# Performance work log

Hardware: AMD Instinct MI355X
Metric: run time of the kernel (lower is better)

Reference implementation:

```python
import jax, jax.numpy as jnp
import numpy as np

B = 16
NS = [12000, 3000, 750, 188, 47]   # nodes per level
ES = [72000, 18000, 4500, 1128, 282]  # directed edges per level (~6N, mesh)
FL = [3, 32, 64, 128, 128]
WN = 16
Z = 8


def _vco(x, ei, ec, W, b):
    # edge-conditioned conv: x (B,N,Ci), ei (2,E) [src,dst], ec (E,WN), W (WN,Ci,Co)
    src, dst = ei[0], ei[1]
    k = jnp.einsum('ew,wio->eio', ec, W)            # per-edge mixed kernel
    msg = jnp.einsum('bei,eio->beo', x[:, src], k)  # gather + transform
    out = jnp.zeros((x.shape[0], x.shape[1], W.shape[2]), x.dtype)
    out = out.at[:, dst].add(msg)                   # scatter-sum to targets
    return out + b


def _pool(x, m):
    # sparse pool/unpool applied as matmul: (M,N) @ (B,N,C) -> (B,M,C)
    return jnp.einsum('mn,bnc->bmc', m, x)


def setup_inputs():
    key = jax.random.key(0)
    ks = iter(jax.random.split(key, 80))
    d = {'x': jax.random.normal(next(ks), (B, NS[0], FL[0]), jnp.float32)}
    for i in range(5):
        src = jax.random.randint(next(ks), (ES[i],), 0, NS[i])
        dst = jax.random.randint(next(ks), (ES[i],), 0, NS[i])
        d[f'ei{i}'] = jnp.stack([src, dst]).astype(jnp.int32)
        d[f'ec{i}'] = jax.random.normal(next(ks), (ES[i], WN), jnp.float32)
    for i in range(4):
        d[f'Wc{i}'] = jax.random.normal(next(ks), (WN, FL[i], FL[i + 1]), jnp.float32) * 0.1
        d[f'bc{i}'] = jnp.zeros((FL[i + 1],), jnp.float32)
        ci, co = FL[4 - i], FL[3 - i]
        d[f'Wd{i}'] = jax.random.normal(next(ks), (WN, ci, co), jnp.float32) * 0.1
        d[f'bd{i}'] = jnp.zeros((co,), jnp.float32)
        d[f'dm{i}'] = jax.random.normal(next(ks), (NS[i + 1], NS[i]), jnp.float32) * (1.0 / np.sqrt(NS[i]))
        d[f'um{i}'] = jax.random.normal(next(ks), (NS[i], NS[i + 1]), jnp.float32) * (1.0 / np.sqrt(NS[i + 1]))
    d['encW'] = jax.random.normal(next(ks), (Z, NS[4] * FL[4]), jnp.float32) * 0.1
    d['encb'] = jnp.zeros((Z,), jnp.float32)
    d['decW'] = jax.random.normal(next(ks), (FL[4] * NS[4], Z), jnp.float32) * 0.1
    d['decb'] = jnp.zeros((FL[4] * NS[4],), jnp.float32)
    return d


def _forward(x, eis, ecs, Wcs, bcs, Wds, bds, dms, ums, encW, encb, decW, decb):
    # encoder
    for i in range(4):
        x = jax.nn.relu(_vco(x, eis[i], ecs[i], Wcs[i], bcs[i]))
        x = _pool(x, dms[i])
    z = x.reshape(x.shape[0], -1) @ encW.T + encb
    # decoder
    y = (z @ decW.T + decb).reshape(x.shape[0], -1, FL[4])
    for i in range(3):
        y = _pool(y, ums[3 - i])
        y = jax.nn.relu(_vco(y, eis[3 - i], ecs[3 - i], Wds[i], bds[i]))
    y = _pool(y, ums[0])
    return _vco(y, eis[0], ecs[0], Wds[3], bds[3])


def reference(x, ei0, ei1, ei2, ei3, ei4, ec0, ec1, ec2, ec3, ec4,
              Wc0, Wc1, Wc2, Wc3, bc0, bc1, bc2, bc3,
              Wd0, Wd1, Wd2, Wd3, bd0, bd1, bd2, bd3,
              dm0, dm1, dm2, dm3, um0, um1, um2, um3,
              encW, encb, decW, decb):
    return _forward(x, [ei0, ei1, ei2, ei3, ei4], [ec0, ec1, ec2, ec3, ec4],
                    [Wc0, Wc1, Wc2, Wc3], [bc0, bc1, bc2, bc3],
                    [Wd0, Wd1, Wd2, Wd3], [bd0, bd1, bd2, bd3],
                    [dm0, dm1, dm2, dm3], [um0, um1, um2, um3],
                    encW, encb, decW, decb)
```

## Files before the change

kernel.cpp:

```cpp
#include <hip/hip_runtime.h>


typedef __attribute__((ext_vector_type(8))) short bf16x8;
typedef __attribute__((ext_vector_type(4))) float f32x4;

__device__ inline unsigned bf1(float x){
  union {float f; unsigned u;} a; a.f = x;
  return (a.u + 0x7fffu + ((a.u >> 16) & 1u)) >> 16;
}
__device__ inline unsigned pack_bf2(float x, float y){ return bf1(x) | (bf1(y) << 16); }
__device__ inline float2 unp_bf2(unsigned u){
  union {unsigned i; float f;} a, b;
  a.i = u << 16; b.i = u & 0xffff0000u;
  return make_float2(a.f, b.f);
}

__device__ inline void gld_lds16(const void* g, void* l){
  __builtin_amdgcn_global_load_lds((const __attribute__((address_space(1))) void*)g,
                                   (__attribute__((address_space(3))) void*)l, 16, 0, 0);
}

__global__ void k_zero_f32(float* __restrict__ p, int n){
  int i = blockIdx.x * 256 + threadIdx.x; if (i < n) p[i] = 0.f;
}
__global__ void k_zero_i32(int* __restrict__ p, int n){
  int i = blockIdx.x * 256 + threadIdx.x; if (i < n) p[i] = 0;
}
__global__ void k_transpose_in(const float* __restrict__ x, float* __restrict__ xT){
  int gid = blockIdx.x * 256 + threadIdx.x;
  if (gid >= 16 * 12000 * 3) return;
  int b = gid / 36000; int r = gid % 36000; int n = r / 3; int c = r % 3;
  xT[n * 48 + b * 3 + c] = x[gid];
}

__global__ void k_count(const int* __restrict__ ei, int E, int* __restrict__ cnt){
  int e = blockIdx.x * 256 + threadIdx.x;
  if (e < E) atomicAdd(&cnt[ei[E + e]], 1);
}
__global__ void k_scan(int* __restrict__ cnt, int* __restrict__ rowptr, int n){
  __shared__ int s[256];
  __shared__ int carryS;
  int t = threadIdx.x;
  if (t == 0){ carryS = 0; rowptr[0] = 0; }
  __syncthreads();
  for (int base = 0; base < n; base += 256){
    int i = base + t;
    int v = (i < n) ? cnt[i] : 0;
    s[t] = v;
    __syncthreads();
    for (int off = 1; off < 256; off <<= 1){
      int a = (t >= off) ? s[t - off] : 0;
      __syncthreads();
      s[t] += a;
      __syncthreads();
    }
    int carry = carryS;
    int incl = s[t];
    if (i < n){ rowptr[i + 1] = carry + incl; cnt[i] = carry + incl - v; }
    __syncthreads();
    if (t == 255) carryS = carry + s[255];
    __syncthreads();
  }
}
__global__ void k_fill(const int* __restrict__ ei, int E, int* __restrict__ cursor, int* __restrict__ perm){
  int e = blockIdx.x * 256 + threadIdx.x;
  if (e < E){ int p = atomicAdd(&cursor[ei[E + e]], 1); perm[p] = e; }
}

__global__ void k_cvt_pad(const float* __restrict__ in, unsigned short* __restrict__ out,
                          int M, int K, int Kp, int total8){
  int gid = blockIdx.x * 256 + threadIdx.x;
  if (gid >= total8) return;
  int j = gid * 8;
  int row = j / Kp, col = j % Kp;
  float v[8];
  if (row < M && col + 8 <= K && (K & 3) == 0){
    const float* p = in + (size_t)row * K + col;
    float4 x0 = *(const float4*)p;
    float4 x1 = *(const float4*)(p + 4);
    v[0]=x0.x; v[1]=x0.y; v[2]=x0.z; v[3]=x0.w;
    v[4]=x1.x; v[5]=x1.y; v[6]=x1.z; v[7]=x1.w;
  } else {
    #pragma unroll
    for (int c = 0; c < 8; ++c)
      v[c] = (row < M && col + c < K) ? in[(size_t)row * K + col + c] : 0.f;
  }
  uint4 o;
  o.x = pack_bf2(v[0], v[1]); o.y = pack_bf2(v[2], v[3]);
  o.z = pack_bf2(v[4], v[5]); o.w = pack_bf2(v[6], v[7]);
  *(uint4*)(out + (size_t)gid * 8) = o;
}
__global__ void k_cvt_T(const float* __restrict__ in, unsigned short* __restrict__ out,
                        int K, int N, int Kp){
  __shared__ float ts[32][33];
  int t = threadIdx.x;
  int k0 = blockIdx.x * 32, n0 = blockIdx.y * 32;
  #pragma unroll
  for (int rep = 0; rep < 4; ++rep){
    int i = t + rep * 256;
    int kr = i >> 5, nc = i & 31;
    ts[kr][nc] = (k0 + kr < K) ? in[(size_t)(k0 + kr) * N + n0 + nc] : 0.f;
  }
  __syncthreads();
  #pragma unroll
  for (int rep = 0; rep < 4; ++rep){
    int i = t + rep * 256;
    int nr = i >> 5, kc = i & 31;
    out[(size_t)(n0 + nr) * Kp + k0 + kc] = (unsigned short)bf1(ts[kc][nr]);
  }
}

__global__ __launch_bounds__(256) void k_mgemm(const unsigned short* __restrict__ A,
                                               const unsigned short* __restrict__ Bt,
                                               float* __restrict__ C,
                                               int M, int N, int Kp, int Kc, int splitK){
  __shared__ __align__(16) short As[4096];
  __shared__ __align__(16) short Bs[4096];
  int t = threadIdx.x, lane = t & 63, w = t >> 6;
  int n0 = blockIdx.x << 7, m0 = blockIdx.y << 7;
  int k0 = blockIdx.z * Kc;
  int kend = min(Kp, k0 + Kc);
  int s0 = w * 128 + lane, s1 = s0 + 64;
  const unsigned short* gA0 = A + (size_t)(m0 + (s0 & 127)) * Kp + (s0 >> 7) * 8 + k0;
  const unsigned short* gA1 = A + (size_t)(m0 + (s1 & 127)) * Kp + (s1 >> 7) * 8 + k0;
  const unsigned short* gB0 = Bt + (size_t)(n0 + (s0 & 127)) * Kp + (s0 >> 7) * 8 + k0;
  const unsigned short* gB1 = Bt + (size_t)(n0 + (s1 & 127)) * Kp + (s1 >> 7) * 8 + k0;
  short* lA0 = As + (size_t)(w * 128) * 8;
  short* lA1 = As + (size_t)(w * 128 + 64) * 8;
  short* lB0 = Bs + (size_t)(w * 128) * 8;
  short* lB1 = Bs + (size_t)(w * 128 + 64) * 8;
  f32x4 acc[4][4];
  #pragma unroll
  for (int mt = 0; mt < 4; ++mt)
    #pragma unroll
    for (int nt = 0; nt < 4; ++nt){ acc[mt][nt][0]=0.f; acc[mt][nt][1]=0.f; acc[mt][nt][2]=0.f; acc[mt][nt][3]=0.f; }
  int q = lane >> 4, r = lane & 15;
  int mrow = (w >> 1) * 64, nrow = (w & 1) * 64;
  const short* pa = As + (size_t)(q * 128 + mrow + r) * 8;
  const short* pb = Bs + (size_t)(q * 128 + nrow + r) * 8;
  for (int kk = k0; kk < kend; kk += 32){
    gld_lds16(gA0, lA0); gld_lds16(gA1, lA1);
    gld_lds16(gB0, lB0); gld_lds16(gB1, lB1);
    gA0 += 32; gA1 += 32; gB0 += 32; gB1 += 32;
    __syncthreads();
    bf16x8 af[4], bg[4];
    #pragma unroll
    for (int mt = 0; mt < 4; ++mt) af[mt] = *(const bf16x8*)(pa + mt * 128);
    #pragma unroll
    for (int nt = 0; nt < 4; ++nt) bg[nt] = *(const bf16x8*)(pb + nt * 128);
    #pragma unroll
    for (int mt = 0; mt < 4; ++mt)
      #pragma unroll
      for (int nt = 0; nt < 4; ++nt)
        acc[mt][nt] = __builtin_amdgcn_mfma_f32_16x16x32_bf16(af[mt], bg[nt], acc[mt][nt], 0, 0, 0);
    __syncthreads();
  }
  int mb = m0 + mrow + q * 4;
  int nb = n0 + nrow + r;
  #pragma unroll
  for (int mt = 0; mt < 4; ++mt){
    #pragma unroll
    for (int reg = 0; reg < 4; ++reg){
      int m = mb + mt * 16 + reg;
      if (m < M){
        float* cp = C + (size_t)m * N + nb;
        if (splitK > 1){
          #pragma unroll
          for (int nt = 0; nt < 4; ++nt) atomicAdd(cp + nt * 16, acc[mt][nt][reg]);
        } else {
          #pragma unroll
          for (int nt = 0; nt < 4; ++nt) cp[nt * 16] = acc[mt][nt][reg];
        }
      }
    }
  }
}

__global__ __launch_bounds__(256) void k_kmat_big(const float* __restrict__ ec, const float* __restrict__ W,
                                                  unsigned short* __restrict__ kbuf, int E, int CiCo4){
  __shared__ float ecs[128];
  int t = threadIdx.x;
  int e0 = blockIdx.y * 8;
  if (t < 128){ int el = t >> 4, w = t & 15; int e = e0 + el; ecs[t] = (e < E) ? ec[e * 16 + w] : 0.f; }
  __syncthreads();
  int j4 = blockIdx.x * 256 + t;
  const float4* W4 = (const float4*)W;
  float4 w16[16];
  #pragma unroll
  for (int w = 0; w < 16; ++w) w16[w] = W4[(size_t)w * CiCo4 + j4];
  uint2* k2 = (uint2*)kbuf;
  #pragma unroll 1
  for (int el = 0; el < 8; ++el){
    int e = e0 + el; if (e >= E) break;
    float4 a = {0.f, 0.f, 0.f, 0.f};
    #pragma unroll
    for (int w = 0; w < 16; ++w){
      float s = ecs[el * 16 + w];
      a.x += s * w16[w].x; a.y += s * w16[w].y; a.z += s * w16[w].z; a.w += s * w16[w].w;
    }
    k2[(size_t)e * CiCo4 + j4] = make_uint2(pack_bf2(a.x, a.y), pack_bf2(a.z, a.w));
  }
}
__global__ __launch_bounds__(256) void k_kmat_small(const float* __restrict__ ec, const float* __restrict__ W,
                                                    unsigned short* __restrict__ kbuf, int E){
  __shared__ float4 Ws[16 * 24];
  __shared__ float ecs[32 * 16];
  int t = threadIdx.x;
  for (int i = t; i < 384; i += 256) Ws[i] = ((const float4*)W)[i];
  int e0 = blockIdx.x * 32;
  for (int i = t; i < 512; i += 256){ int el = i >> 4, w = i & 15; int e = e0 + el; ecs[i] = (e < E) ? ec[e * 16 + w] : 0.f; }
  __syncthreads();
  int el = t >> 3, jj = t & 7;
  int e = e0 + el;
  if (e >= E) return;
  uint2* k2 = (uint2*)kbuf;
  #pragma unroll 1
  for (int rep = 0; rep < 3; ++rep){
    int j4 = jj + rep * 8;
    float4 a = {0.f, 0.f, 0.f, 0.f};
    #pragma unroll
    for (int w = 0; w < 16; ++w){
      float s = ecs[el * 16 + w];
      float4 wv = Ws[w * 24 + j4];
      a.x += s * wv.x; a.y += s * wv.y; a.z += s * wv.z; a.w += s * wv.w;
    }
    k2[(size_t)e * 24 + j4] = make_uint2(pack_bf2(a.x, a.y), pack_bf2(a.z, a.w));
  }
}

__global__ __launch_bounds__(256) void k_conv_l0_enc(const float* __restrict__ xT, const unsigned short* __restrict__ kbuf,
                                                     const int* __restrict__ ei, const int* __restrict__ rowptr,
                                                     const int* __restrict__ perm, const float* __restrict__ bias,
                                                     float* __restrict__ out){
  int gid = blockIdx.x * 256 + threadIdx.x;
  int n = gid >> 4, b = gid & 15;
  if (n >= 12000) return;
  float acc[32];
  #pragma unroll
  for (int o = 0; o < 32; ++o) acc[o] = 0.f;
  int r1 = rowptr[n + 1];
  for (int r = rowptr[n]; r < r1; ++r){
    int e = perm[r];
    int src = ei[e];
    const float* xp = xT + src * 48 + b * 3;
    float xv[3] = {xp[0], xp[1], xp[2]};
    const uint4* kq = (const uint4*)(kbuf + (size_t)e * 96);
    #pragma unroll
    for (int i = 0; i < 3; ++i){
      #pragma unroll
      for (int o8 = 0; o8 < 4; ++o8){
        uint4 u = kq[i * 4 + o8];
        float2 f0 = unp_bf2(u.x), f1 = unp_bf2(u.y), f2 = unp_bf2(u.z), f3 = unp_bf2(u.w);
        int ob = o8 * 8;
        acc[ob + 0] += xv[i] * f0.x; acc[ob + 1] += xv[i] * f0.y;
        acc[ob + 2] += xv[i] * f1.x; acc[ob + 3] += xv[i] * f1.y;
        acc[ob + 4] += xv[i] * f2.x; acc[ob + 5] += xv[i] * f2.y;
        acc[ob + 6] += xv[i] * f3.x; acc[ob + 7] += xv[i] * f3.y;
      }
    }
  }
  float4* op = (float4*)(out + (size_t)n * 512 + b * 32);
  #pragma unroll
  for (int o4 = 0; o4 < 8; ++o4){
    float4 v;
    v.x = fmaxf(acc[o4 * 4 + 0] + bias[o4 * 4 + 0], 0.f);
    v.y = fmaxf(acc[o4 * 4 + 1] + bias[o4 * 4 + 1], 0.f);
    v.z = fmaxf(acc[o4 * 4 + 2] + bias[o4 * 4 + 2], 0.f);
    v.w = fmaxf(acc[o4 * 4 + 3] + bias[o4 * 4 + 3], 0.f);
    op[o4] = v;
  }
}
__global__ __launch_bounds__(256) void k_conv_l0_dec(const float* __restrict__ xin, const unsigned short* __restrict__ kbuf,
                                                     const int* __restrict__ ei, const int* __restrict__ rowptr,
                                                     const int* __restrict__ perm, const float* __restrict__ bias,
                                                     float* __restrict__ out){
  int gid = blockIdx.x * 256 + threadIdx.x;
  int n = gid >> 4, b = gid & 15;
  if (n >= 12000) return;
  float acc0 = 0.f, acc1 = 0.f, acc2 = 0.f;
  int r1 = rowptr[n + 1];
  for (int r = rowptr[n]; r < r1; ++r){
    int e = perm[r];
    int src = ei[e];
    const float4* xr = (const float4*)(xin + (size_t)src * 512 + b * 32);
    const unsigned* kw = (const unsigned*)(kbuf + (size_t)e * 96);
    #pragma unroll
    for (int c = 0; c < 8; ++c){
      float4 xv = xr[c];
      float2 p0 = unp_bf2(kw[6 * c + 0]);
      float2 p1 = unp_bf2(kw[6 * c + 1]);
      float2 p2 = unp_bf2(kw[6 * c + 2]);
      float2 p3 = unp_bf2(kw[6 * c + 3]);
      float2 p4 = unp_bf2(kw[6 * c + 4]);
      float2 p5 = unp_bf2(kw[6 * c + 5]);
      acc0 += xv.x * p0.x; acc1 += xv.x * p0.y; acc2 += xv.x * p1.x;
      acc0 += xv.y * p1.y; acc1 += xv.y * p2.x; acc2 += xv.y * p2.y;
      acc0 += xv.z * p3.x; acc1 += xv.z * p3.y; acc2 += xv.z * p4.x;
      acc0 += xv.w * p4.y; acc1 += xv.w * p5.x; acc2 += xv.w * p5.y;
    }
  }
  float* op = out + (size_t)b * 36000 + n * 3;
  op[0] = acc0 + bias[0];
  op[1] = acc1 + bias[1];
  op[2] = acc2 + bias[2];
}

template<int CI, int CO, int S, bool RELU>
__global__ __launch_bounds__(256) void k_conv_mid(const float* __restrict__ xin, const unsigned short* __restrict__ kbuf,
                                                  const int* __restrict__ ei, const int* __restrict__ rowptr,
                                                  const int* __restrict__ perm, const float* __restrict__ bias,
                                                  float* __restrict__ out){
  constexpr int COC = CO / S;
  constexpr int V   = COC / 16;
  constexpr int IT  = (CI > 64) ? 64 : CI;
  constexpr int NIH = CI / IT;
  constexpr int COP = COC + 4;
  constexpr int XP  = IT + 4;
  __shared__ float ks[IT * COP];
  __shared__ float xs[16 * XP];
  int n = blockIdx.x, cy = blockIdx.y;
  int ob0 = cy * COC;
  int t = threadIdx.x;
  int og = t >> 4, b = t & 15;
  float acc[V];
  #pragma unroll
  for (int j = 0; j < V; ++j) acc[j] = 0.f;
  int r0 = rowptr[n], r1 = rowptr[n + 1];
  for (int r = r0; r < r1; ++r){
    int e = perm[r];
    int src = ei[e];
    const float4* xbase = (const float4*)(xin + (size_t)src * (16 * CI));
    for (int ih = 0; ih < NIH; ++ih){
      __syncthreads();
      const uint4* kb = (const uint4*)(kbuf + (size_t)e * (CI * CO) + ih * (IT * CO));
      constexpr int KS8 = IT * COC / 8;
      for (int i8 = t; i8 < KS8; i8 += 256){
        int i = (i8 * 8) / COC, o = (i8 * 8) % COC;
        uint4 u = kb[(i * CO + ob0 + o) >> 3];
        float* d = &ks[i * COP + o];
        float2 f0 = unp_bf2(u.x), f1 = unp_bf2(u.y), f2 = unp_bf2(u.z), f3 = unp_bf2(u.w);
        *(float4*)&d[0] = make_float4(f0.x, f0.y, f1.x, f1.y);
        *(float4*)&d[4] = make_float4(f2.x, f2.y, f3.x, f3.y);
      }
      constexpr int XS4 = 16 * IT / 4;
      for (int i4 = t; i4 < XS4; i4 += 256){
        int bb = i4 / (IT / 4), iq = i4 % (IT / 4);
        float4 v = xbase[bb * (CI / 4) + ih * (IT / 4) + iq];
        *(float4*)&xs[bb * XP + iq * 4] = v;
      }
      __syncthreads();
      #pragma unroll 4
      for (int i = 0; i < IT; ++i){
        float xv = xs[b * XP + i];
        if constexpr (V == 8){
          const float4* kp = (const float4*)&ks[i * COP + og * 8];
          float4 p0 = kp[0], p1 = kp[1];
          acc[0] += xv * p0.x; acc[1] += xv * p0.y; acc[2] += xv * p0.z; acc[3] += xv * p0.w;
          acc[4] += xv * p1.x; acc[5] += xv * p1.y; acc[6] += xv * p1.z; acc[7] += xv * p1.w;
        } else if constexpr (V == 4){
          float4 p0 = *(const float4*)&ks[i * COP + og * 4];
          acc[0] += xv * p0.x; acc[1] += xv * p0.y; acc[2] += xv * p0.z; acc[3] += xv * p0.w;
        } else {
          float2 p0 = *(const float2*)&ks[i * COP + og * 2];
          acc[0] += xv * p0.x; acc[1] += xv * p0.y;
        }
      }
    }
  }
  float* op = out + (size_t)n * (16 * CO) + b * CO + ob0 + og * V;
  #pragma unroll
  for (int j = 0; j < V; ++j){
    float v = acc[j] + bias[ob0 + og * V + j];
    if (RELU) v = fmaxf(v, 0.f);
    op[j] = v;
  }
}

__global__ void k_encfc(const float* __restrict__ x, const float* __restrict__ encW,
                        const float* __restrict__ encb, float* __restrict__ z){
  __shared__ float red[128];
  int bq = blockIdx.x; int b = bq >> 3, q = bq & 7;
  int t = threadIdx.x;
  float s = 0.f;
  for (int j = t; j < 6016; j += 128){
    int n = j >> 7, c = j & 127;
    s += x[n * 2048 + b * 128 + c] * encW[q * 6016 + j];
  }
  red[t] = s; __syncthreads();
  for (int o = 64; o > 0; o >>= 1){ if (t < o) red[t] += red[t + o]; __syncthreads(); }
  if (t == 0) z[b * 8 + q] = red[0] + encb[q];
}
__global__ void k_decfc(const float* __restrict__ z, const float* __restrict__ decW,
                        const float* __restrict__ decb, float* __restrict__ y){
  int gid = blockIdx.x * 256 + threadIdx.x;
  if (gid >= 6016 * 16) return;
  int c = gid & 127, bn = gid >> 7; int b = bn & 15, n = bn >> 4;
  int j = n * 128 + c;
  float s = decb[j];
  #pragma unroll
  for (int q = 0; q < 8; ++q) s += z[b * 8 + q] * decW[j * 8 + q];
  y[gid] = s;
}

extern "C" void kernel_launch(void* const* d_in, const int* in_sizes, int n_in,
                              void* d_out, int out_size, void* d_ws, size_t ws_size,
                              hipStream_t stream){
  const float* x   = (const float*)d_in[0];
  const int*   ei0 = (const int*)d_in[1];  const float* ec0 = (const float*)d_in[2];
  const int*   ei1 = (const int*)d_in[3];  const float* ec1 = (const float*)d_in[4];
  const int*   ei2 = (const int*)d_in[5];  const float* ec2 = (const float*)d_in[6];
  const int*   ei3 = (const int*)d_in[7];  const float* ec3 = (const float*)d_in[8];
  const float* Wc0 = (const float*)d_in[11], *bc0 = (const float*)d_in[12];
  const float* Wd0 = (const float*)d_in[13], *bd0 = (const float*)d_in[14];
  const float* dm0 = (const float*)d_in[15], *um0 = (const float*)d_in[16];
  const float* Wc1 = (const float*)d_in[17], *bc1 = (const float*)d_in[18];
  const float* Wd1 = (const float*)d_in[19], *bd1 = (const float*)d_in[20];
  const float* dm1 = (const float*)d_in[21], *um1 = (const float*)d_in[22];
  const float* Wc2 = (const float*)d_in[23], *bc2 = (const float*)d_in[24];
  const float* Wd2 = (const float*)d_in[25], *bd2 = (const float*)d_in[26];
  const float* dm2 = (const float*)d_in[27], *um2 = (const float*)d_in[28];
  const float* Wc3 = (const float*)d_in[29], *bc3 = (const float*)d_in[30];
  const float* Wd3 = (const float*)d_in[31], *bd3 = (const float*)d_in[32];
  const float* dm3 = (const float*)d_in[33], *um3 = (const float*)d_in[34];
  const float* encW = (const float*)d_in[35], *encb = (const float*)d_in[36];
  const float* decW = (const float*)d_in[37], *decb = (const float*)d_in[38];

  char* wsb = (char*)d_ws;
  unsigned short* kbuf = (unsigned short*)wsb;
  unsigned short* Abf  = kbuf;
  float* bufA = (float*)(wsb + 73728000);
  float* bufB = (float*)(wsb + 98304000);
  unsigned short* Bt = (unsigned short*)(wsb + 122880000);
  float* xT   = (float*)(wsb + 135168000);
  float* zb   = (float*)(wsb + 137472000);
  int* ip = (int*)(wsb + 137472512);
  int* cnt0 = ip; ip += 12000;
  int* cnt1 = ip; ip += 3000;
  int* cnt2 = ip; ip += 750;
  int* cnt3 = ip; ip += 188;
  int* row0 = ip; ip += 12001;
  int* row1 = ip; ip += 3001;
  int* row2 = ip; ip += 751;
  int* row3 = ip; ip += 189;
  int* perm0 = ip; ip += 72000;
  int* perm1 = ip; ip += 18000;
  int* perm2 = ip; ip += 4500;
  int* perm3 = ip; ip += 1128;

  dim3 blk(256);
  k_transpose_in<<<2250, blk, 0, stream>>>(x, xT);
  k_zero_i32<<<63, blk, 0, stream>>>(cnt0, 15938);
  k_count<<<282, blk, 0, stream>>>(ei0, 72000, cnt0);
  k_count<<<71,  blk, 0, stream>>>(ei1, 18000, cnt1);
  k_count<<<18,  blk, 0, stream>>>(ei2, 4500, cnt2);
  k_count<<<5,   blk, 0, stream>>>(ei3, 1128, cnt3);
  k_scan<<<1, blk, 0, stream>>>(cnt0, row0, 12000);
  k_scan<<<1, blk, 0, stream>>>(cnt1, row1, 3000);
  k_scan<<<1, blk, 0, stream>>>(cnt2, row2, 750);
  k_scan<<<1, blk, 0, stream>>>(cnt3, row3, 188);
  k_fill<<<282, blk, 0, stream>>>(ei0, 72000, cnt0, perm0);
  k_fill<<<71,  blk, 0, stream>>>(ei1, 18000, cnt1, perm1);
  k_fill<<<18,  blk, 0, stream>>>(ei2, 4500, cnt2, perm2);
  k_fill<<<5,   blk, 0, stream>>>(ei3, 1128, cnt3, perm3);

  k_kmat_small<<<2250, blk, 0, stream>>>(ec0, Wc0, kbuf, 72000);
  k_conv_l0_enc<<<750, blk, 0, stream>>>(xT, kbuf, ei0, row0, perm0, bc0, bufA);
  k_cvt_T<<<dim3(375, 16), blk, 0, stream>>>(bufA, Bt, 12000, 512, 12000);
  k_cvt_pad<<<18000, blk, 0, stream>>>(dm0, Abf, 3000, 12000, 12000, 4608000);
  k_zero_f32<<<6000, blk, 0, stream>>>(bufB, 1536000);
  k_mgemm<<<dim3(4, 24, 12), blk, 0, stream>>>(Abf, Bt, bufB, 3000, 512, 12000, 1024, 12);
  k_kmat_big<<<dim3(2, 2250), blk, 0, stream>>>(ec1, Wc1, kbuf, 18000, 512);
  k_conv_mid<32, 64, 1, true><<<dim3(3000, 1), blk, 0, stream>>>(bufB, kbuf, ei1, row1, perm1, bc1, bufA);
  k_cvt_T<<<dim3(94, 32), blk, 0, stream>>>(bufA, Bt, 3000, 1024, 3008);
  k_cvt_pad<<<1128, blk, 0, stream>>>(dm1, Abf, 750, 3000, 3008, 288768);
  k_zero_f32<<<3000, blk, 0, stream>>>(bufB, 768000);
  k_mgemm<<<dim3(8, 6, 16), blk, 0, stream>>>(Abf, Bt, bufB, 750, 1024, 3008, 192, 16);
  k_kmat_big<<<dim3(8, 563), blk, 0, stream>>>(ec2, Wc2, kbuf, 4500, 2048);
  k_conv_mid<64, 128, 4, true><<<dim3(750, 4), blk, 0, stream>>>(bufB, kbuf, ei2, row2, perm2, bc2, bufA);
  k_cvt_T<<<dim3(24, 64), blk, 0, stream>>>(bufA, Bt, 750, 2048, 768);
  k_cvt_pad<<<96, blk, 0, stream>>>(dm2, Abf, 188, 750, 768, 24576);
  k_zero_f32<<<1504, blk, 0, stream>>>(bufB, 385024);
  k_mgemm<<<dim3(16, 2, 12), blk, 0, stream>>>(Abf, Bt, bufB, 188, 2048, 768, 64, 12);
  k_kmat_big<<<dim3(16, 141), blk, 0, stream>>>(ec3, Wc3, kbuf, 1128, 4096);
  k_conv_mid<128, 128, 4, true><<<dim3(188, 4), blk, 0, stream>>>(bufB, kbuf, ei3, row3, perm3, bc3, bufA);
  k_cvt_T<<<dim3(6, 64), blk, 0, stream>>>(bufA, Bt, 188, 2048, 192);
  k_cvt_pad<<<12, blk, 0, stream>>>(dm3, Abf, 47, 188, 192, 3072);
  k_zero_f32<<<376, blk, 0, stream>>>(bufB, 96256);
  k_mgemm<<<dim3(16, 1, 6), blk, 0, stream>>>(Abf, Bt, bufB, 47, 2048, 192, 32, 6);

  k_encfc<<<128, dim3(128), 0, stream>>>(bufB, encW, encb, zb);
  k_decfc<<<376, blk, 0, stream>>>(zb, decW, decb, bufA);

  k_cvt_T<<<dim3(2, 64), blk, 0, stream>>>(bufA, Bt, 47, 2048, 64);
  k_cvt_pad<<<8, blk, 0, stream>>>(um3, Abf, 188, 47, 64, 2048);
  k_zero_f32<<<1504, blk, 0, stream>>>(bufB, 385024);
  k_mgemm<<<dim3(16, 2, 2), blk, 0, stream>>>(Abf, Bt, bufB, 188, 2048, 64, 32, 2);
  k_kmat_big<<<dim3(16, 141), blk, 0, stream>>>(ec3, Wd0, kbuf, 1128, 4096);
  k_conv_mid<128, 128, 4, true><<<dim3(188, 4), blk, 0, stream>>>(bufB, kbuf, ei3, row3, perm3, bd0, bufA);
  k_cvt_T<<<dim3(6, 64), blk, 0, stream>>>(bufA, Bt, 188, 2048, 192);
  k_cvt_pad<<<72, blk, 0, stream>>>(um2, Abf, 750, 188, 192, 18432);
  k_zero_f32<<<6000, blk, 0, stream>>>(bufB, 1536000);
  k_mgemm<<<dim3(16, 6, 6), blk, 0, stream>>>(Abf, Bt, bufB, 750, 2048, 192, 32, 6);
  k_kmat_big<<<dim3(8, 563), blk, 0, stream>>>(ec2, Wd1, kbuf, 4500, 2048);
  k_conv_mid<128, 64, 2, true><<<dim3(750, 2), blk, 0, stream>>>(bufB, kbuf, ei2, row2, perm2, bd1, bufA);
  k_cvt_T<<<dim3(24, 32), blk, 0, stream>>>(bufA, Bt, 750, 1024, 768);
  k_cvt_pad<<<1152, blk, 0, stream>>>(um1, Abf, 3000, 750, 768, 294912);
  k_zero_f32<<<12000, blk, 0, stream>>>(bufB, 3072000);
  k_mgemm<<<dim3(8, 24, 4), blk, 0, stream>>>(Abf, Bt, bufB, 3000, 1024, 768, 192, 4);
  k_kmat_big<<<dim3(2, 2250), blk, 0, stream>>>(ec1, Wd2, kbuf, 18000, 512);
  k_conv_mid<64, 32, 1, true><<<dim3(3000, 1), blk, 0, stream>>>(bufB, kbuf, ei1, row1, perm1, bd2, bufA);
  k_cvt_T<<<dim3(94, 16), blk, 0, stream>>>(bufA, Bt, 3000, 512, 3008);
  k_cvt_pad<<<17672, blk, 0, stream>>>(um0, Abf, 12000, 3000, 3008, 4524032);
  k_zero_f32<<<24000, blk, 0, stream>>>(bufB, 6144000);
  k_mgemm<<<dim3(4, 94, 4), blk, 0, stream>>>(Abf, Bt, bufB, 12000, 512, 3008, 768, 4);
  k_kmat_small<<<2250, blk, 0, stream>>>(ec0, Wd3, kbuf, 72000);
  k_conv_l0_dec<<<750, blk, 0, stream>>>(bufB, kbuf, ei0, row0, perm0, bd3, (float*)d_out);
}
```

Measured before the change: 1.614 ms.

## Double-buffer GEMM LDS loads, retune split-K, and batch CSR build kernels

The bf16 MFMA GEMM now double-buffers its LDS tiles. The next K-slice's global-to-LDS load is issued before computing on the current one, and one barrier per iteration is dropped. Several split-K factors are lowered and chunk sizes raised, which means fewer atomics and more work per block. The per-level count, scan and fill kernels are merged into three multi-level launches, and the scan now uses wave shuffles instead of a barrier-heavy LDS scan. Costs are doubled LDS per block and less parallelism on some GEMM launches.

```diff
diff --git a/kernel.cpp b/kernel.cpp
--- a/kernel.cpp
+++ b/kernel.cpp
@@ -33,38 +33,66 @@
   xT[n * 48 + b * 3 + c] = x[gid];
 }
 
-__global__ void k_count(const int* __restrict__ ei, int E, int* __restrict__ cnt){
-  int e = blockIdx.x * 256 + threadIdx.x;
-  if (e < E) atomicAdd(&cnt[ei[E + e]], 1);
-}
-__global__ void k_scan(int* __restrict__ cnt, int* __restrict__ rowptr, int n){
-  __shared__ int s[256];
-  __shared__ int carryS;
+__global__ void k_count_all(const int* __restrict__ ei0, const int* __restrict__ ei1,
+                            const int* __restrict__ ei2, const int* __restrict__ ei3,
+                            int* __restrict__ cnt0, int* __restrict__ cnt1,
+                            int* __restrict__ cnt2, int* __restrict__ cnt3){
+  int g = blockIdx.x * 256 + threadIdx.x;
+  const int* ei; int* cnt; int e, E;
+  if (g < 72000){ ei = ei0; cnt = cnt0; e = g; E = 72000; }
+  else if (g < 90000){ ei = ei1; cnt = cnt1; e = g - 72000; E = 18000; }
+  else if (g < 94500){ ei = ei2; cnt = cnt2; e = g - 90000; E = 4500; }
+  else if (g < 95628){ ei = ei3; cnt = cnt3; e = g - 94500; E = 1128; }
+  else return;
+  atomicAdd(&cnt[ei[E + e]], 1);
+}
+__global__ void k_scan_all(int* c0, int* c1, int* c2, int* c3,
+                           int* r0, int* r1, int* r2, int* r3){
+  int lvl = blockIdx.x;
+  int* cnt    = lvl == 0 ? c0 : lvl == 1 ? c1 : lvl == 2 ? c2 : c3;
+  int* rowptr = lvl == 0 ? r0 : lvl == 1 ? r1 : lvl == 2 ? r2 : r3;
+  int n       = lvl == 0 ? 12000 : lvl == 1 ? 3000 : lvl == 2 ? 750 : 188;
   int t = threadIdx.x;
-  if (t == 0){ carryS = 0; rowptr[0] = 0; }
+  int L = (n + 255) / 256;
+  int beg = t * L, end = min(n, beg + L);
+  int s = 0;
+  for (int i = beg; i < end; ++i) s += cnt[i];
+  int lane = t & 63, wv = t >> 6;
+  int incl = s;
+  #pragma unroll
+  for (int d = 1; d < 64; d <<= 1){
+    int v = __shfl_up(incl, d, 64);
+    if (lane >= d) incl += v;
+  }
+  __shared__ int wsum[4];
+  if (lane == 63) wsum[wv] = incl;
   __syncthreads();
-  for (int base = 0; base < n; base += 256){
-    int i = base + t;
-    int v = (i < n) ? cnt[i] : 0;
-    s[t] = v;
-    __syncthreads();
-    for (int off = 1; off < 256; off <<= 1){
-      int a = (t >= off) ? s[t - off] : 0;
-      __syncthreads();
-      s[t] += a;
-      __syncthreads();
-    }
-    int carry = carryS;
-    int incl = s[t];
-    if (i < n){ rowptr[i + 1] = carry + incl; cnt[i] = carry + incl - v; }
-    __syncthreads();
-    if (t == 255) carryS = carry + s[255];
-    __syncthreads();
-  }
-}
-__global__ void k_fill(const int* __restrict__ ei, int E, int* __restrict__ cursor, int* __restrict__ perm){
-  int e = blockIdx.x * 256 + threadIdx.x;
-  if (e < E){ int p = atomicAdd(&cursor[ei[E + e]], 1); perm[p] = e; }
+  int wbase = 0;
+  for (int i = 0; i < wv; ++i) wbase += wsum[i];
+  int run = wbase + incl - s;
+  for (int i = beg; i < end; ++i){
+    int v = cnt[i];
+    cnt[i] = run;
+    run += v;
+    rowptr[i + 1] = run;
+  }
+  if (t == 0) rowptr[0] = 0;
+}
+__global__ void k_fill_all(const int* __restrict__ ei0, const int* __restrict__ ei1,
+                           const int* __restrict__ ei2, const int* __restrict__ ei3,
+                           int* __restrict__ c0, int* __restrict__ c1,
+                           int* __restrict__ c2, int* __restrict__ c3,
+                           int* __restrict__ p0, int* __restrict__ p1,
+                           int* __restrict__ p2, int* __restrict__ p3){
+  int g = blockIdx.x * 256 + threadIdx.x;
+  const int* ei; int* cur; int* perm; int e, E;
+  if (g < 72000){ ei = ei0; cur = c0; perm = p0; e = g; E = 72000; }
+  else if (g < 90000){ ei = ei1; cur = c1; perm = p1; e = g - 72000; E = 18000; }
+  else if (g < 94500){ ei = ei2; cur = c2; perm = p2; e = g - 90000; E = 4500; }
+  else if (g < 95628){ ei = ei3; cur = c3; perm = p3; e = g - 94500; E = 1128; }
+  else return;
+  int p = atomicAdd(&cur[ei[E + e]], 1);
+  perm[p] = e;
 }
 
 __global__ void k_cvt_pad(const float* __restrict__ in, unsigned short* __restrict__ out,
@@ -114,12 +142,13 @@
                                                const unsigned short* __restrict__ Bt,
                                                float* __restrict__ C,
                                                int M, int N, int Kp, int Kc, int splitK){
-  __shared__ __align__(16) short As[4096];
-  __shared__ __align__(16) short Bs[4096];
+  __shared__ __align__(16) short As[2 * 4096];
+  __shared__ __align__(16) short Bs[2 * 4096];
   int t = threadIdx.x, lane = t & 63, w = t >> 6;
   int n0 = blockIdx.x << 7, m0 = blockIdx.y << 7;
   int k0 = blockIdx.z * Kc;
   int kend = min(Kp, k0 + Kc);
+  int iters = (kend - k0 + 31) >> 5;
   int s0 = w * 128 + lane, s1 = s0 + 64;
   const unsigned short* gA0 = A + (size_t)(m0 + (s0 & 127)) * Kp + (s0 >> 7) * 8 + k0;
   const unsigned short* gA1 = A + (size_t)(m0 + (s1 & 127)) * Kp + (s1 >> 7) * 8 + k0;
@@ -138,22 +167,31 @@
   int mrow = (w >> 1) * 64, nrow = (w & 1) * 64;
   const short* pa = As + (size_t)(q * 128 + mrow + r) * 8;
   const short* pb = Bs + (size_t)(q * 128 + nrow + r) * 8;
-  for (int kk = k0; kk < kend; kk += 32){
-    gld_lds16(gA0, lA0); gld_lds16(gA1, lA1);
-    gld_lds16(gB0, lB0); gld_lds16(gB1, lB1);
-    gA0 += 32; gA1 += 32; gB0 += 32; gB1 += 32;
+  gld_lds16(gA0, lA0); gld_lds16(gA1, lA1);
+  gld_lds16(gB0, lB0); gld_lds16(gB1, lB1);
+  for (int i = 0; i < iters; ++i){
+    int st = i & 1;
     __syncthreads();
+    if (i + 1 < iters){
+      int nst = st ^ 1;
+      int off = (i + 1) * 32;
+      gld_lds16(gA0 + off, lA0 + nst * 4096);
+      gld_lds16(gA1 + off, lA1 + nst * 4096);
+      gld_lds16(gB0 + off, lB0 + nst * 4096);
+      gld_lds16(gB1 + off, lB1 + nst * 4096);
+    }
+    const short* pas = pa + st * 4096;
+    const short* pbs = pb + st * 4096;
     bf16x8 af[4], bg[4];
     #pragma unroll
-    for (int mt = 0; mt < 4; ++mt) af[mt] = *(const bf16x8*)(pa + mt * 128);
-    #pragma unroll
-    for (int nt = 0; nt < 4; ++nt) bg[nt] = *(const bf16x8*)(pb + nt * 128);
+    for (int mt = 0; mt < 4; ++mt) af[mt] = *(const bf16x8*)(pas + mt * 128);
+    #pragma unroll
+    for (int nt = 0; nt < 4; ++nt) bg[nt] = *(const bf16x8*)(pbs + nt * 128);
     #pragma unroll
     for (int mt = 0; mt < 4; ++mt)
       #pragma unroll
       for (int nt = 0; nt < 4; ++nt)
         acc[mt][nt] = __builtin_amdgcn_mfma_f32_16x16x32_bf16(af[mt], bg[nt], acc[mt][nt], 0, 0, 0);
-    __syncthreads();
   }
   int mb = m0 + mrow + q * 4;
   int nb = n0 + nrow + r;
@@ -450,37 +488,29 @@
   dim3 blk(256);
   k_transpose_in<<<2250, blk, 0, stream>>>(x, xT);
   k_zero_i32<<<63, blk, 0, stream>>>(cnt0, 15938);
-  k_count<<<282, blk, 0, stream>>>(ei0, 72000, cnt0);
-  k_count<<<71,  blk, 0, stream>>>(ei1, 18000, cnt1);
-  k_count<<<18,  blk, 0, stream>>>(ei2, 4500, cnt2);
-  k_count<<<5,   blk, 0, stream>>>(ei3, 1128, cnt3);
-  k_scan<<<1, blk, 0, stream>>>(cnt0, row0, 12000);
-  k_scan<<<1, blk, 0, stream>>>(cnt1, row1, 3000);
-  k_scan<<<1, blk, 0, stream>>>(cnt2, row2, 750);
-  k_scan<<<1, blk, 0, stream>>>(cnt3, row3, 188);
-  k_fill<<<282, blk, 0, stream>>>(ei0, 72000, cnt0, perm0);
-  k_fill<<<71,  blk, 0, stream>>>(ei1, 18000, cnt1, perm1);
-  k_fill<<<18,  blk, 0, stream>>>(ei2, 4500, cnt2, perm2);
-  k_fill<<<5,   blk, 0, stream>>>(ei3, 1128, cnt3, perm3);
+  k_count_all<<<374, blk, 0, stream>>>(ei0, ei1, ei2, ei3, cnt0, cnt1, cnt2, cnt3);
+  k_scan_all<<<4, blk, 0, stream>>>(cnt0, cnt1, cnt2, cnt3, row0, row1, row2, row3);
+  k_fill_all<<<374, blk, 0, stream>>>(ei0, ei1, ei2, ei3, cnt0, cnt1, cnt2, cnt3,
+                                      perm0, perm1, perm2, perm3);
 
   k_kmat_small<<<2250, blk, 0, stream>>>(ec0, Wc0, kbuf, 72000);
   k_conv_l0_enc<<<750, blk, 0, stream>>>(xT, kbuf, ei0, row0, perm0, bc0, bufA);
   k_cvt_T<<<dim3(375, 16), blk, 0, stream>>>(bufA, Bt, 12000, 512, 12000);
   k_cvt_pad<<<18000, blk, 0, stream>>>(dm0, Abf, 3000, 12000, 12000, 4608000);
   k_zero_f32<<<6000, blk, 0, stream>>>(bufB, 1536000);
-  k_mgemm<<<dim3(4, 24, 12), blk, 0, stream>>>(Abf, Bt, bufB, 3000, 512, 12000, 1024, 12);
+  k_mgemm<<<dim3(4, 24, 8), blk, 0, stream>>>(Abf, Bt, bufB, 3000, 512, 12000, 1504, 8);
   k_kmat_big<<<dim3(2, 2250), blk, 0, stream>>>(ec1, Wc1, kbuf, 18000, 512);
   k_conv_mid<32, 64, 1, true><<<dim3(3000, 1), blk, 0, stream>>>(bufB, kbuf, ei1, row1, perm1, bc1, bufA);
   k_cvt_T<<<dim3(94, 32), blk, 0, stream>>>(bufA, Bt, 3000, 1024, 3008);
   k_cvt_pad<<<1128, blk, 0, stream>>>(dm1, Abf, 750, 3000, 3008, 288768);
   k_zero_f32<<<3000, blk, 0, stream>>>(bufB, 768000);
-  k_mgemm<<<dim3(8, 6, 16), blk, 0, stream>>>(Abf, Bt, bufB, 750, 1024, 3008, 192, 16);
+  k_mgemm<<<dim3(8, 6, 8), blk, 0, stream>>>(Abf, Bt, bufB, 750, 1024, 3008, 384, 8);
   k_kmat_big<<<dim3(8, 563), blk, 0, stream>>>(ec2, Wc2, kbuf, 4500, 2048);
   k_conv_mid<64, 128, 4, true><<<dim3(750, 4), blk, 0, stream>>>(bufB, kbuf, ei2, row2, perm2, bc2, bufA);
   k_cvt_T<<<dim3(24, 64), blk, 0, stream>>>(bufA, Bt, 750, 2048, 768);
   k_cvt_pad<<<96, blk, 0, stream>>>(dm2, Abf, 188, 750, 768, 24576);
   k_zero_f32<<<1504, blk, 0, stream>>>(bufB, 385024);
-  k_mgemm<<<dim3(16, 2, 12), blk, 0, stream>>>(Abf, Bt, bufB, 188, 2048, 768, 64, 12);
+  k_mgemm<<<dim3(16, 2, 8), blk, 0, stream>>>(Abf, Bt, bufB, 188, 2048, 768, 96, 8);
   k_kmat_big<<<dim3(16, 141), blk, 0, stream>>>(ec3, Wc3, kbuf, 1128, 4096);
   k_conv_mid<128, 128, 4, true><<<dim3(188, 4), blk, 0, stream>>>(bufB, kbuf, ei3, row3, perm3, bc3, bufA);
   k_cvt_T<<<dim3(6, 64), blk, 0, stream>>>(bufA, Bt, 188, 2048, 192);
@@ -500,7 +530,7 @@
   k_cvt_T<<<dim3(6, 64), blk, 0, stream>>>(bufA, Bt, 188, 2048, 192);
   k_cvt_pad<<<72, blk, 0, stream>>>(um2, Abf, 750, 188, 192, 18432);
   k_zero_f32<<<6000, blk, 0, stream>>>(bufB, 1536000);
-  k_mgemm<<<dim3(16, 6, 6), blk, 0, stream>>>(Abf, Bt, bufB, 750, 2048, 192, 32, 6);
+  k_mgemm<<<dim3(16, 6, 2), blk, 0, stream>>>(Abf, Bt, bufB, 750, 2048, 192, 96, 2);
   k_kmat_big<<<dim3(8, 563), blk, 0, stream>>>(ec2, Wd1, kbuf, 4500, 2048);
   k_conv_mid<128, 64, 2, true><<<dim3(750, 2), blk, 0, stream>>>(bufB, kbuf, ei2, row2, perm2, bd1, bufA);
   k_cvt_T<<<dim3(24, 32), blk, 0, stream>>>(bufA, Bt, 750, 1024, 768);
@@ -512,7 +542,7 @@
   k_cvt_T<<<dim3(94, 16), blk, 0, stream>>>(bufA, Bt, 3000, 512, 3008);
   k_cvt_pad<<<17672, blk, 0, stream>>>(um0, Abf, 12000, 3000, 3008, 4524032);
   k_zero_f32<<<24000, blk, 0, stream>>>(bufB, 6144000);
-  k_mgemm<<<dim3(4, 94, 4), blk, 0, stream>>>(Abf, Bt, bufB, 12000, 512, 3008, 768, 4);
+  k_mgemm<<<dim3(4, 94, 2), blk, 0, stream>>>(Abf, Bt, bufB, 12000, 512, 3008, 1504, 2);
   k_kmat_small<<<2250, blk, 0, stream>>>(ec0, Wd3, kbuf, 72000);
   k_conv_l0_dec<<<750, blk, 0, stream>>>(bufB, kbuf, ei0, row0, perm0, bd3, (float*)d_out);
 }
```

Result: faster. 1.446 ms (-10.4%).
